# Performance work log

Hardware: AMD Instinct MI355X
Metric: run time of the kernel (lower is better)

## Reference

```python
import jax, jax.numpy as jnp
import numpy as np

BATCH = 8192          # per-modality batch size; n = 2*BATCH
FEAT = 128            # feature dim (kept small -> memory-bound n^2 distance matrix)
NUM_IDS = 1000
MARGIN = 0.3


def setup_inputs() -> dict:
    key = jax.random.key(0)
    k1, k2 = jax.random.split(key)
    n = 2 * BATCH
    inputs = jax.random.normal(k1, (n, FEAT), dtype=jnp.float32)
    # same identity set in both modality halves -> cross-modal positives exist per row
    t = jax.random.randint(k2, (BATCH,), 0, NUM_IDS, dtype=jnp.int32)
    targets = jnp.concatenate([t, t], axis=0)
    return {"inputs": inputs, "targets": targets}


def reference(inputs, targets):
    n = inputs.shape[0]
    # pairwise euclidean distances: ||xi||^2 + ||xj||^2 - 2 xi.xj
    sq = jnp.sum(inputs * inputs, axis=1)                      # [n]
    d2 = sq[:, None] + sq[None, :] - 2.0 * (inputs @ inputs.T)  # [n, n]
    dist = jnp.sqrt(jnp.clip(d2, 1e-12, None))
    # modality: first half 0, second half 1; self.sub selects CROSS-modality pairs
    modality = jnp.arange(n) >= (n // 2)
    cross = modality[:, None] != modality[None, :]              # [n, n] bool
    same = targets[:, None] == targets[None, :]                 # same identity
    pos = same & cross        # mask1: same label, different modality
    neg = (~same) & cross     # mask2: diff label, different modality
    # masked hard mining: per-row max over positives, min over negatives
    dist_ap = jnp.max(jnp.where(pos, dist, -jnp.inf), axis=1)   # [n]
    dist_an = jnp.min(jnp.where(neg, dist, jnp.inf), axis=1)    # [n]
    # MarginRankingLoss with y=1: mean(relu(-(dist_an - dist_ap) + margin))
    loss = jnp.mean(jax.nn.relu(dist_ap - dist_an + MARGIN))
    correct = jnp.sum(dist_an >= dist_ap).astype(jnp.int32)
    return (loss, correct)
```

## Files before the change

### kernel.cpp

```cpp
#include <hip/hip_runtime.h>

#define N_TOTAL 16384
#define HALF    8192
#define FEAT    128
#define MARGIN  0.3f
#define NBINS   1024

typedef __attribute__((ext_vector_type(8))) short  short8v;
typedef __attribute__((ext_vector_type(4))) float  float4v;

__device__ __forceinline__ unsigned short f32_to_bf16_rne(float f) {
    unsigned u = __float_as_uint(f);
    u += 0x7FFFu + ((u >> 16) & 1u);
    return (unsigned short)(u >> 16);
}

template<int CTRL>
__device__ __forceinline__ float dpp_mov_f(float x) {
    return __int_as_float(__builtin_amdgcn_update_dpp(
        0, __float_as_int(x), CTRL, 0xF, 0xF, true));
}
__device__ __forceinline__ float rowmin16(float x) {
    x = fminf(x, dpp_mov_f<0xB1>(x));
    x = fminf(x, dpp_mov_f<0x4E>(x));
    x = fminf(x, dpp_mov_f<0x141>(x));
    x = fminf(x, dpp_mov_f<0x140>(x));
    return x;
}
__device__ __forceinline__ float rowmax16(float x) {
    x = fmaxf(x, dpp_mov_f<0xB1>(x));
    x = fmaxf(x, dpp_mov_f<0x4E>(x));
    x = fmaxf(x, dpp_mov_f<0x141>(x));
    x = fmaxf(x, dpp_mov_f<0x140>(x));
    return x;
}

__global__ __launch_bounds__(1024) void histscan_kernel(
        const int* __restrict__ targets, int* __restrict__ cursor,
        int* __restrict__ accs ) {
    __shared__ int lhist[NBINS];
    const int h = blockIdx.x;
    const int t = threadIdx.x;
    lhist[t] = 0;
    __syncthreads();
    const int* tg = targets + (h << 13);
    #pragma unroll
    for (int k = 0; k < 8; ++k)
        atomicAdd(&lhist[tg[k * 1024 + t]], 1);
    __syncthreads();
    const int lane = t & 63, wave = t >> 6;
    int x = lhist[t];
    const int orig = x;
    #pragma unroll
    for (int m = 1; m < 64; m <<= 1) {
        int v = __shfl_up(x, m, 64);
        if (lane >= m) x += v;
    }
    __shared__ int wsum[16];
    if (lane == 63) wsum[wave] = x;
    __syncthreads();
    if (t == 0) {
        int s = 0;
        for (int w = 0; w < 16; ++w) { int v = wsum[w]; wsum[w] = s; s += v; }
        if (h == 0) { accs[0] = 0; accs[1] = 0; accs[2] = 0; }
    }
    __syncthreads();
    cursor[(h << 10) + t] = x - orig + wsum[wave];
}

__global__ __launch_bounds__(256) void prep_kernel(
        const float* __restrict__ X, const int* __restrict__ targets,
        int* __restrict__ cursor,
        unsigned* __restrict__ Xb, float* __restrict__ sq, int* __restrict__ labs) {
    const int wave = threadIdx.x >> 6, lane = threadIdx.x & 63;
    const int src = blockIdx.x * 4 + wave;
    const int h   = src >> 13;
    const int lbl = targets[src];
    int dst;
    if (lane == 0)
        dst = (h << 13) + atomicAdd(&cursor[(h << 10) + lbl], 1);
    dst = __shfl(dst, 0, 64);
    const float2 xv = ((const float2*)(X + (size_t)src * FEAT))[lane];
    unsigned short h0 = f32_to_bf16_rne(xv.x);
    unsigned short h1 = f32_to_bf16_rne(xv.y);
    Xb[(dst >> 4) * 1024 + (lane >> 2) * 64 + (dst & 15) * 4 + (lane & 3)] =
        (unsigned)h0 | ((unsigned)h1 << 16);
    float x0 = __uint_as_float((unsigned)h0 << 16);
    float x1 = __uint_as_float((unsigned)h1 << 16);
    float p = x0 * x0 + x1 * x1;
    #pragma unroll
    for (int m = 1; m < 64; m <<= 1) p += __shfl_xor(p, m, 64);
    if (lane == 0) {
        sq[dst]   = p;
        labs[dst] = lbl;
    }
}

__global__ __launch_bounds__(256, 2) void cross_kernel(
        const unsigned short* __restrict__ Xb, const float* __restrict__ sq,
        const int* __restrict__ labs,
        float* __restrict__ pmin, float* __restrict__ pmax) {
    const int t = threadIdx.x;
    const int wave = t >> 6, lane = t & 63;
    const int q = lane >> 4, c = lane & 15;
    const int b    = blockIdx.x;
    const int pass = b >> 8;
    const int bb   = b & 255;
    const int cc   = bb & 7;
    const int rt   = (bb >> 3) * 4 + wave;
    const int own  = pass ? HALF : 0;
    const int oth  = pass ? 0 : HALF;
    const int ownbase = own + rt * 64;

    const uint4* XbV = (const uint4*)Xb;

    const float NEG_INF = __int_as_float((int)0xFF800000u);
    const float POS_INF = __int_as_float(0x7F800000);

    short8v af[4][4];
    const int pA0 = ownbase >> 4;
    #pragma unroll
    for (int ti = 0; ti < 4; ++ti)
        #pragma unroll
        for (int kk = 0; kk < 4; ++kk)
            af[ti][kk] = *(const short8v*)&XbV[(pA0 + ti) * 256 + kk * 64 + lane];

    const int aMin = labs[ownbase], aMax = labs[ownbase + 63];

    float rmin[16], rmax[16];
    #pragma unroll
    for (int i = 0; i < 16; ++i) { rmin[i] = POS_INF; rmax[i] = NEG_INF; }

    for (int tile = 0; tile < 16; ++tile) {
        const int colbase = oth + cc * 1024 + tile * 64;
        const int bMn = labs[colbase], bMx = labs[colbase + 63];
        const bool overlap = (aMax >= bMn) && (bMx >= aMin);

        #pragma unroll
        for (int hh = 0; hh < 2; ++hh) {
            const int sub = colbase + hh * 32;
            const int pB0 = sub >> 4;
            short8v bfr[2][4];
            #pragma unroll
            for (int tj = 0; tj < 2; ++tj)
                #pragma unroll
                for (int kk = 0; kk < 4; ++kk)
                    bfr[tj][kk] = *(const short8v*)&XbV[(pB0 + tj) * 256 + kk * 64 + lane];
            float sB[2];
            #pragma unroll
            for (int tj = 0; tj < 2; ++tj)
                sB[tj] = sq[sub + tj * 16 + c];

            float4v acc[4][2] = {};
            #pragma unroll
            for (int kk = 0; kk < 4; ++kk)
                #pragma unroll
                for (int ti = 0; ti < 4; ++ti)
                    #pragma unroll
                    for (int tj = 0; tj < 2; ++tj)
                        acc[ti][tj] = __builtin_amdgcn_mfma_f32_16x16x32_bf16(
                            af[ti][kk], bfr[tj][kk], acc[ti][tj], 0, 0, 0);

            if (!overlap) {
                #pragma unroll
                for (int ti = 0; ti < 4; ++ti)
                    #pragma unroll
                    for (int tj = 0; tj < 2; ++tj)
                        #pragma unroll
                        for (int reg = 0; reg < 4; ++reg) {
                            float v = fmaf(acc[ti][tj][reg], -2.0f, sB[tj]);
                            rmin[ti * 4 + reg] = fminf(rmin[ti * 4 + reg], v);
                        }
            } else {
                int tB[2];
                #pragma unroll
                for (int tj = 0; tj < 2; ++tj)
                    tB[tj] = labs[sub + tj * 16 + c];
                int tA[16];
                #pragma unroll
                for (int ti = 0; ti < 4; ++ti)
                    #pragma unroll
                    for (int reg = 0; reg < 4; ++reg)
                        tA[ti * 4 + reg] = labs[ownbase + ti * 16 + q * 4 + reg];
                #pragma unroll
                for (int ti = 0; ti < 4; ++ti)
                    #pragma unroll
                    for (int tj = 0; tj < 2; ++tj)
                        #pragma unroll
                        for (int reg = 0; reg < 4; ++reg) {
                            int ri = ti * 4 + reg;
                            float v = fmaf(acc[ti][tj][reg], -2.0f, sB[tj]);
                            bool same = (tA[ri] == tB[tj]);
                            rmin[ri] = fminf(rmin[ri], same ? POS_INF : v);
                            rmax[ri] = fmaxf(rmax[ri], same ? v : NEG_INF);
                        }
            }
        }
    }

    #pragma unroll
    for (int i = 0; i < 16; ++i) {
        rmin[i] = rowmin16(rmin[i]);
        rmax[i] = rowmax16(rmax[i]);
    }
    if (c == 0) {
        #pragma unroll
        for (int ti = 0; ti < 4; ++ti)
            #pragma unroll
            for (int reg = 0; reg < 4; ++reg) {
                int gi = ownbase + ti * 16 + q * 4 + reg;
                float sA = sq[gi];
                pmin[cc * N_TOTAL + gi] = sA + rmin[ti * 4 + reg];
                pmax[cc * N_TOTAL + gi] = sA + rmax[ti * 4 + reg];
            }
    }
}

__global__ __launch_bounds__(256) void final_kernel(
        const float* __restrict__ pmin, const float* __restrict__ pmax,
        int* __restrict__ accs ,
        float* __restrict__ out) {
    const int i = blockIdx.x * 256 + threadIdx.x;
    const int t = threadIdx.x;
    float* accF = (float*)&accs[0];
    int*   accI = &accs[1];
    int*   tick = &accs[2];
    float an2 = pmin[i], ap2 = pmax[i];
    #pragma unroll
    for (int ccp = 1; ccp < 8; ++ccp) {
        an2 = fminf(an2, pmin[ccp * N_TOTAL + i]);
        ap2 = fmaxf(ap2, pmax[ccp * N_TOTAL + i]);
    }
    float ap = sqrtf(fmaxf(ap2, 1e-12f));
    float an = sqrtf(fmaxf(an2, 1e-12f));
    float term = fmaxf(ap - an + MARGIN, 0.0f);
    int cnt = (an >= ap) ? 1 : 0;
    #pragma unroll
    for (int m = 1; m < 64; m <<= 1) {
        term += __shfl_xor(term, m, 64);
        cnt  += __shfl_xor(cnt, m, 64);
    }
    __shared__ float sf[4];
    __shared__ int   si[4];
    if ((t & 63) == 0) { sf[t >> 6] = term; si[t >> 6] = cnt; }
    __syncthreads();
    if (t == 0) {
        atomicAdd(accF, sf[0] + sf[1] + sf[2] + sf[3]);
        atomicAdd(accI, si[0] + si[1] + si[2] + si[3]);
        __threadfence();
        int old = atomicAdd(tick, 1);
        if (old == gridDim.x - 1) {
            __threadfence();
            float S = atomicAdd(accF, 0.0f);
            int   C = atomicAdd(accI, 0);
            out[0] = S / (float)N_TOTAL;
            out[1] = (float)C;
        }
    }
}

extern "C" void kernel_launch(void* const* d_in, const int* in_sizes, int n_in,
                              void* d_out, int out_size, void* d_ws, size_t ws_size,
                              hipStream_t stream) {
    const float* X       = (const float*)d_in[0];
    const int*   targets = (const int*)d_in[1];
    float* out = (float*)d_out;

    char* ws = (char*)d_ws;
    const size_t XB_BYTES = (size_t)N_TOTAL * FEAT * 2;
    unsigned* Xb  = (unsigned*)ws;
    float* sq     = (float*)(ws + XB_BYTES);
    int* labs     = (int*)(ws + XB_BYTES + 1 * 65536);
    float* pmin   = (float*)(ws + XB_BYTES + 2 * 65536);
    float* pmax   = (float*)(ws + XB_BYTES + 2 * 65536 + 8 * N_TOTAL * 4);
    int* cursor   = (int*)(ws + XB_BYTES + 2 * 65536 + 16 * N_TOTAL * 4);
    int* accs     = cursor + 2 * NBINS;

    histscan_kernel<<<2, 1024, 0, stream>>>(targets, cursor, accs);
    prep_kernel    <<<4096, 256, 0, stream>>>(X, targets, cursor, Xb, sq, labs);
    cross_kernel   <<<512, 256, 0, stream>>>(
        (const unsigned short*)Xb, sq, labs, pmin, pmax);
    final_kernel   <<<64, 256, 0, stream>>>(pmin, pmax, accs, out);
}
```

Baseline: 111.6 us.

## Exploit distance symmetry: compute one cross block, reduce rows and columns

The cross-modal distance block is symmetric, so the kernel now computes only the first-half-rows by second-half-columns block once instead of two passes. Each tile yields both row min/max and column min/max, with column partials written per row tile and reduced in the final kernel. B tiles are staged into LDS through double-buffered global_load_lds. This halves the MFMA work but adds column shuffles, larger partial buffers (128 partials per column) and a heavier final reduction.

```diff
diff --git a/kernel.cpp b/kernel.cpp
--- a/kernel.cpp
+++ b/kernel.cpp
@@ -99,18 +99,18 @@
 __global__ __launch_bounds__(256, 2) void cross_kernel(
         const unsigned short* __restrict__ Xb, const float* __restrict__ sq,
         const int* __restrict__ labs,
-        float* __restrict__ pmin, float* __restrict__ pmax) {
+        float* __restrict__ prow_min, float* __restrict__ prow_max,
+        float* __restrict__ pcol_min, float* __restrict__ pcol_max) {
+    __shared__ unsigned Bs[2][2048];
     const int t = threadIdx.x;
     const int wave = t >> 6, lane = t & 63;
     const int q = lane >> 4, c = lane & 15;
-    const int b    = blockIdx.x;
-    const int pass = b >> 8;
-    const int bb   = b & 255;
-    const int cc   = bb & 7;
-    const int rt   = (bb >> 3) * 4 + wave;
-    const int own  = pass ? HALF : 0;
-    const int oth  = pass ? 0 : HALF;
-    const int ownbase = own + rt * 64;
+    const int b  = blockIdx.x;
+    const int rg = b >> 4;
+    const int cc = b & 15;
+    const int rt = rg * 4 + wave;
+    const int rowbase = rt * 64;
+    const int chunk0  = HALF + cc * 512;
 
     const uint4* XbV = (const uint4*)Xb;
 
@@ -118,82 +118,114 @@
     const float POS_INF = __int_as_float(0x7F800000);
 
     short8v af[4][4];
-    const int pA0 = ownbase >> 4;
+    const int pA0 = rowbase >> 4;
     #pragma unroll
     for (int ti = 0; ti < 4; ++ti)
         #pragma unroll
         for (int kk = 0; kk < 4; ++kk)
             af[ti][kk] = *(const short8v*)&XbV[(pA0 + ti) * 256 + kk * 64 + lane];
 
-    const int aMin = labs[ownbase], aMax = labs[ownbase + 63];
+    const int aMin = labs[rowbase], aMax = labs[rowbase + 63];
+
+    float sAv[16]; int tA[16];
+    #pragma unroll
+    for (int ti = 0; ti < 4; ++ti)
+        #pragma unroll
+        for (int reg = 0; reg < 4; ++reg) {
+            sAv[ti * 4 + reg] = sq[rowbase + ti * 16 + q * 4 + reg];
+            tA[ti * 4 + reg]  = labs[rowbase + ti * 16 + q * 4 + reg];
+        }
 
     float rmin[16], rmax[16];
     #pragma unroll
     for (int i = 0; i < 16; ++i) { rmin[i] = POS_INF; rmax[i] = NEG_INF; }
 
-    for (int tile = 0; tile < 16; ++tile) {
-        const int colbase = oth + cc * 1024 + tile * 64;
-        const int bMn = labs[colbase], bMx = labs[colbase + 63];
-        const bool overlap = (aMax >= bMn) && (bMx >= aMin);
-
-        #pragma unroll
-        for (int hh = 0; hh < 2; ++hh) {
-            const int sub = colbase + hh * 32;
-            const int pB0 = sub >> 4;
-            short8v bfr[2][4];
-            #pragma unroll
-            for (int tj = 0; tj < 2; ++tj)
-                #pragma unroll
-                for (int kk = 0; kk < 4; ++kk)
-                    bfr[tj][kk] = *(const short8v*)&XbV[(pB0 + tj) * 256 + kk * 64 + lane];
-            float sB[2];
-            #pragma unroll
-            for (int tj = 0; tj < 2; ++tj)
-                sB[tj] = sq[sub + tj * 16 + c];
-
-            float4v acc[4][2] = {};
+    auto stage = [&](int s, int buf) {
+        const unsigned* gsrc = (const unsigned*)Xb
+                             + (size_t)((chunk0 + s * 32) >> 4) * 1024;
+        #pragma unroll
+        for (int p = 0; p < 2; ++p)
+            __builtin_amdgcn_global_load_lds(
+                (const __attribute__((address_space(1))) void*)(gsrc + p * 1024 + t * 4),
+                (__attribute__((address_space(3))) void*)(&Bs[buf][p * 1024 + t * 4]),
+                16, 0, 0);
+    };
+
+    stage(0, 0);
+    for (int s = 0; s < 16; ++s) {
+        __syncthreads();
+        if (s + 1 < 16) stage(s + 1, (s + 1) & 1);
+
+        const int sub = chunk0 + s * 32;
+        const unsigned* Bb = &Bs[s & 1][0];
+
+        short8v bfr[2][4];
+        #pragma unroll
+        for (int tj = 0; tj < 2; ++tj)
             #pragma unroll
             for (int kk = 0; kk < 4; ++kk)
-                #pragma unroll
-                for (int ti = 0; ti < 4; ++ti)
-                    #pragma unroll
-                    for (int tj = 0; tj < 2; ++tj)
-                        acc[ti][tj] = __builtin_amdgcn_mfma_f32_16x16x32_bf16(
-                            af[ti][kk], bfr[tj][kk], acc[ti][tj], 0, 0, 0);
-
-            if (!overlap) {
-                #pragma unroll
-                for (int ti = 0; ti < 4; ++ti)
-                    #pragma unroll
-                    for (int tj = 0; tj < 2; ++tj)
-                        #pragma unroll
-                        for (int reg = 0; reg < 4; ++reg) {
-                            float v = fmaf(acc[ti][tj][reg], -2.0f, sB[tj]);
-                            rmin[ti * 4 + reg] = fminf(rmin[ti * 4 + reg], v);
-                        }
-            } else {
-                int tB[2];
+                bfr[tj][kk] = *(const short8v*)&Bb[tj * 1024 + kk * 256 + lane * 4];
+        float sB[2] = { sq[sub + c], sq[sub + 16 + c] };
+        const bool overlap = (aMax >= labs[sub]) && (labs[sub + 31] >= aMin);
+
+        float4v acc[4][2] = {};
+        #pragma unroll
+        for (int kk = 0; kk < 4; ++kk)
+            #pragma unroll
+            for (int ti = 0; ti < 4; ++ti)
                 #pragma unroll
                 for (int tj = 0; tj < 2; ++tj)
-                    tB[tj] = labs[sub + tj * 16 + c];
-                int tA[16];
+                    acc[ti][tj] = __builtin_amdgcn_mfma_f32_16x16x32_bf16(
+                        af[ti][kk], bfr[tj][kk], acc[ti][tj], 0, 0, 0);
+
+        float cmin[2] = { POS_INF, POS_INF };
+        float cmax[2] = { NEG_INF, NEG_INF };
+
+        if (!overlap) {
+            #pragma unroll
+            for (int ti = 0; ti < 4; ++ti)
                 #pragma unroll
-                for (int ti = 0; ti < 4; ++ti)
+                for (int tj = 0; tj < 2; ++tj)
                     #pragma unroll
-                    for (int reg = 0; reg < 4; ++reg)
-                        tA[ti * 4 + reg] = labs[ownbase + ti * 16 + q * 4 + reg];
+                    for (int reg = 0; reg < 4; ++reg) {
+                        int ri = ti * 4 + reg;
+                        float tv = fmaf(acc[ti][tj][reg], -2.0f, sB[tj]);
+                        float uv = fmaf(acc[ti][tj][reg], -2.0f, sAv[ri]);
+                        rmin[ri] = fminf(rmin[ri], tv);
+                        cmin[tj] = fminf(cmin[tj], uv);
+                    }
+        } else {
+            int tB[2] = { labs[sub + c], labs[sub + 16 + c] };
+            #pragma unroll
+            for (int ti = 0; ti < 4; ++ti)
                 #pragma unroll
-                for (int ti = 0; ti < 4; ++ti)
+                for (int tj = 0; tj < 2; ++tj)
                     #pragma unroll
-                    for (int tj = 0; tj < 2; ++tj)
-                        #pragma unroll
-                        for (int reg = 0; reg < 4; ++reg) {
-                            int ri = ti * 4 + reg;
-                            float v = fmaf(acc[ti][tj][reg], -2.0f, sB[tj]);
-                            bool same = (tA[ri] == tB[tj]);
-                            rmin[ri] = fminf(rmin[ri], same ? POS_INF : v);
-                            rmax[ri] = fmaxf(rmax[ri], same ? v : NEG_INF);
-                        }
+                    for (int reg = 0; reg < 4; ++reg) {
+                        int ri = ti * 4 + reg;
+                        float tv = fmaf(acc[ti][tj][reg], -2.0f, sB[tj]);
+                        float uv = fmaf(acc[ti][tj][reg], -2.0f, sAv[ri]);
+                        bool same = (tA[ri] == tB[tj]);
+                        rmin[ri] = fminf(rmin[ri], same ? POS_INF : tv);
+                        rmax[ri] = fmaxf(rmax[ri], same ? tv : NEG_INF);
+                        cmin[tj] = fminf(cmin[tj], same ? POS_INF : uv);
+                        cmax[tj] = fmaxf(cmax[tj], same ? uv : NEG_INF);
+                    }
+        }
+
+        #pragma unroll
+        for (int m = 16; m <= 32; m <<= 1)
+            #pragma unroll
+            for (int tj = 0; tj < 2; ++tj) {
+                cmin[tj] = fminf(cmin[tj], __shfl_xor(cmin[tj], m, 64));
+                cmax[tj] = fmaxf(cmax[tj], __shfl_xor(cmax[tj], m, 64));
+            }
+        if (q == 0) {
+            #pragma unroll
+            for (int tj = 0; tj < 2; ++tj) {
+                int lc = (sub - HALF) + tj * 16 + c;
+                pcol_min[rt * HALF + lc] = sB[tj] + cmin[tj];
+                pcol_max[rt * HALF + lc] = sB[tj] + cmax[tj];
             }
         }
     }
@@ -208,16 +240,17 @@
         for (int ti = 0; ti < 4; ++ti)
             #pragma unroll
             for (int reg = 0; reg < 4; ++reg) {
-                int gi = ownbase + ti * 16 + q * 4 + reg;
-                float sA = sq[gi];
-                pmin[cc * N_TOTAL + gi] = sA + rmin[ti * 4 + reg];
-                pmax[cc * N_TOTAL + gi] = sA + rmax[ti * 4 + reg];
+                int gr = rowbase + ti * 16 + q * 4 + reg;
+                float sA = sAv[ti * 4 + reg];
+                prow_min[cc * HALF + gr] = sA + rmin[ti * 4 + reg];
+                prow_max[cc * HALF + gr] = sA + rmax[ti * 4 + reg];
             }
     }
 }
 
 __global__ __launch_bounds__(256) void final_kernel(
-        const float* __restrict__ pmin, const float* __restrict__ pmax,
+        const float* __restrict__ prow_min, const float* __restrict__ prow_max,
+        const float* __restrict__ pcol_min, const float* __restrict__ pcol_max,
         int* __restrict__ accs ,
         float* __restrict__ out) {
     const int i = blockIdx.x * 256 + threadIdx.x;
@@ -225,11 +258,23 @@
     float* accF = (float*)&accs[0];
     int*   accI = &accs[1];
     int*   tick = &accs[2];
-    float an2 = pmin[i], ap2 = pmax[i];
-    #pragma unroll
-    for (int ccp = 1; ccp < 8; ++ccp) {
-        an2 = fminf(an2, pmin[ccp * N_TOTAL + i]);
-        ap2 = fmaxf(ap2, pmax[ccp * N_TOTAL + i]);
+
+    float an2, ap2;
+    if (i < HALF) {
+        an2 = prow_min[i]; ap2 = prow_max[i];
+        #pragma unroll
+        for (int p = 1; p < 16; ++p) {
+            an2 = fminf(an2, prow_min[p * HALF + i]);
+            ap2 = fmaxf(ap2, prow_max[p * HALF + i]);
+        }
+    } else {
+        const int lc = i - HALF;
+        an2 = pcol_min[lc]; ap2 = pcol_max[lc];
+        #pragma unroll 8
+        for (int p = 1; p < 128; ++p) {
+            an2 = fminf(an2, pcol_min[p * HALF + lc]);
+            ap2 = fmaxf(ap2, pcol_max[p * HALF + lc]);
+        }
     }
     float ap = sqrtf(fmaxf(ap2, 1e-12f));
     float an = sqrtf(fmaxf(an2, 1e-12f));
@@ -268,17 +313,21 @@
 
     char* ws = (char*)d_ws;
     const size_t XB_BYTES = (size_t)N_TOTAL * FEAT * 2;
-    unsigned* Xb  = (unsigned*)ws;
-    float* sq     = (float*)(ws + XB_BYTES);
-    int* labs     = (int*)(ws + XB_BYTES + 1 * 65536);
-    float* pmin   = (float*)(ws + XB_BYTES + 2 * 65536);
-    float* pmax   = (float*)(ws + XB_BYTES + 2 * 65536 + 8 * N_TOTAL * 4);
-    int* cursor   = (int*)(ws + XB_BYTES + 2 * 65536 + 16 * N_TOTAL * 4);
-    int* accs     = cursor + 2 * NBINS;
+    unsigned* Xb    = (unsigned*)ws;
+    float* sq       = (float*)(ws + XB_BYTES);
+    int* labs       = (int*)(ws + XB_BYTES + 65536);
+    char* p         = ws + XB_BYTES + 2 * 65536;
+    float* prow_min = (float*)p;                      p += 16  * HALF * 4;
+    float* prow_max = (float*)p;                      p += 16  * HALF * 4;
+    float* pcol_min = (float*)p;                      p += 128 * HALF * 4;
+    float* pcol_max = (float*)p;                      p += 128 * HALF * 4;
+    int* cursor     = (int*)p;                        p += 2 * NBINS * 4;
+    int* accs       = (int*)p;
 
     histscan_kernel<<<2, 1024, 0, stream>>>(targets, cursor, accs);
     prep_kernel    <<<4096, 256, 0, stream>>>(X, targets, cursor, Xb, sq, labs);
     cross_kernel   <<<512, 256, 0, stream>>>(
-        (const unsigned short*)Xb, sq, labs, pmin, pmax);
-    final_kernel   <<<64, 256, 0, stream>>>(pmin, pmax, accs, out);
-}
+        (const unsigned short*)Xb, sq, labs, prow_min, prow_max, pcol_min, pcol_max);
+    final_kernel   <<<64, 256, 0, stream>>>(
+        prow_min, prow_max, pcol_min, pcol_max, accs, out);
+}
```

Measured after the change: 116.3 us. +4.2%, slower.
